# Kernel optimization log

Measured on AMD Instinct MI355X. Metric: run time of the kernel, lower is better.

## Reference

```python
import jax, jax.numpy as jnp
import numpy as np

B, D_IN, U, M = 8192, 512, 256, 50  # batch, input_size, num_units(=v_size), max_n_msgs


def _w(key, shape, scale=0.02):
    return (jax.random.normal(key, shape, dtype=jnp.float32) * scale)


def setup_inputs() -> dict:
    key = jax.random.key(0)
    ks = jax.random.split(key, 32)
    inp = {
        "X": jax.random.normal(ks[0], (B, D_IN), dtype=jnp.float32),
        "S": jax.random.normal(ks[1], (B, M, U), dtype=jnp.float32),
        "h": jax.random.normal(ks[2], (B, U), dtype=jnp.float32),
        "v": jax.random.normal(ks[3], (B, U), dtype=jnp.float32),
        # attention params
        "W_sa": _w(ks[4], (U, U)), "W_ha": _w(ks[5], (U, U)),
        "b_a": jnp.zeros((U,), jnp.float32), "v_a": _w(ks[6], (U,)),
        # gates
        "W_f": _w(ks[7], (U, U)), "W_hf": _w(ks[8], (U, U)), "b_f": jnp.zeros((U,), jnp.float32),
        "W_o": _w(ks[9], (U, U)), "W_ho": _w(ks[10], (U, U)), "b_o": jnp.zeros((U,), jnp.float32),
        "W_t": _w(ks[11], (U, U)), "W_ht": _w(ks[12], (U, U)), "b_t": jnp.zeros((U,), jnp.float32),
        "W_k": _w(ks[13], (D_IN, U)), "W_hk": _w(ks[14], (U, U)), "W_vk": _w(ks[15], (U, U)), "b_k": jnp.zeros((U,), jnp.float32),
        "W_s": _w(ks[16], (D_IN, U)), "W_hs": _w(ks[17], (U, U)), "b_s": jnp.zeros((U,), jnp.float32),
        "W_v": _w(ks[18], (U, U)), "W_hv": _w(ks[19], (U, U)), "b_v": jnp.zeros((U,), jnp.float32),
    }
    return inp


def reference(X, S, h, v,
              W_sa, W_ha, b_a, v_a,
              W_f, W_hf, b_f,
              W_o, W_ho, b_o,
              W_t, W_ht, b_t,
              W_k, W_hk, W_vk, b_k,
              W_s, W_hs, b_s,
              W_v, W_hv, b_v):
    # additive attention over messages: a [B, M, U]
    a = jnp.tanh(jnp.einsum('bmv,vu->bmu', S, W_sa) + (h @ W_ha + b_a)[:, None, :])
    scores = jnp.einsum('bmu,u->bm', a, v_a)            # [B, M]
    P = jax.nn.softmax(scores, axis=1)                  # [B, M]
    text = jnp.einsum('bm,bmv->bv', P, S)               # [B, U]
    # LSTM-like gates
    F = jax.nn.sigmoid(text @ W_f + h @ W_hf + b_f)
    O = jax.nn.sigmoid(text @ W_o + h @ W_ho + b_o)
    text_new = jnp.tanh(text @ W_t + h @ W_ht + b_t)
    V = F * v + O * text_new                            # [B, U]
    k = jax.nn.sigmoid(X @ W_k + h @ W_hk + V @ W_vk + b_k)
    hx = jnp.tanh(X @ W_s + h @ W_hs + b_s)
    hv = jnp.tanh(V @ W_v + h @ W_hv + b_v)
    H = (1.0 - k) * hv + k * hx                         # [B, U]
    # original returns (H, P, MSINStateTuple(H, V)); new_state.h == H
    return (H, P, V)
```

## Files before the change

### kernel.cpp

```cpp
#include <hip/hip_runtime.h>
#include <cstddef>

typedef __bf16 bf16x8 __attribute__((ext_vector_type(8)));
typedef unsigned short u16x8 __attribute__((ext_vector_type(8)));
typedef float f32x4 __attribute__((ext_vector_type(4)));

#define B_N 8192
#define M_N 50
#define R_N (B_N * M_N)
#define P_OFF ((size_t)B_N * 256)
#define V_OFF ((size_t)B_N * 256 + (size_t)B_N * 50)
#define NBAT 16
#define NBLK (B_N / NBAT)

__device__ __forceinline__ float bf2f(unsigned short u) {
  return __uint_as_float(((unsigned int)u) << 16);
}
__device__ __forceinline__ unsigned short f2bf(float f) {
  unsigned int u = __float_as_uint(f);
  u += 0x7fffu + ((u >> 16) & 1u);
  return (unsigned short)(u >> 16);
}
__device__ __forceinline__ float fsig(float x) { return 1.f / (1.f + __expf(-x)); }
__device__ __forceinline__ float ftanh(float x) {
  float e = __expf(2.f * x);
  return 1.f - 2.f / (e + 1.f);
}

__device__ __forceinline__ float ld_ext(const void* p, size_t i, bool f32) {
  return f32 ? ((const float*)p)[i] : bf2f(((const unsigned short*)p)[i]);
}

__device__ __forceinline__ void gload_lds16(const void* g, void* l) {
  __builtin_amdgcn_global_load_lds(
      (const __attribute__((address_space(1))) unsigned int*)g,
      (__attribute__((address_space(3))) unsigned int*)l, 16, 0, 0);
}

__device__ __forceinline__ unsigned swz(unsigned a) {
  return a ^ (((a >> 7) & 7u) << 4);
}

__global__ void probe_dtype(const void* __restrict__ X, int* __restrict__ flag) {
  const int lane = threadIdx.x;
  const unsigned short u = ((const unsigned short*)X)[lane * 2];
  const int e = (u >> 7) & 0xff;
  const bool plausible = (e >= 110 && e <= 144) || (u == 0);
  const unsigned long long m = __ballot(plausible);
  if (lane == 0) *flag = (__popcll(m) < 32) ? 1 : 0;
}

struct TJobs {
  const void* src[15];
  unsigned short* dst[15];
  int K[15];
};

__global__ __launch_bounds__(256) void transpose_weights(TJobs jobs, const int* __restrict__ flagp) {
  const bool f32 = *flagp != 0;
  const int z = blockIdx.z;
  const void* __restrict__ src = jobs.src[z];
  unsigned short* __restrict__ dst = jobs.dst[z];
  const int K = jobs.K[z];
  const int k0 = blockIdx.y * 16;
  if (k0 >= K) return;
  const int n0 = blockIdx.x * 16;
  __shared__ __align__(16) unsigned short tile[16][17];
  const int tx = threadIdx.x & 15, ty = threadIdx.x >> 4;
  const size_t sidx = (size_t)(k0 + ty) * 256 + n0 + tx;
  tile[ty][tx] = f32 ? f2bf(((const float*)src)[sidx]) : ((const unsigned short*)src)[sidx];
  __syncthreads();
  dst[(size_t)(n0 + ty) * K + k0 + tx] = tile[tx][ty];
}

struct GJob {
  const void* A[3];
  const unsigned short* Wt[3];
  int K[3];
  int atag[3];
  const void* bias;
  const unsigned short* add;
  unsigned short* out;
  int act;
};
struct GJobs { GJob j[4]; };

__global__ __launch_bounds__(256) void gemm_small(GJobs jobs, const int* __restrict__ flagp) {
  const bool flag32 = *flagp != 0;
  const GJob job = jobs.j[blockIdx.z];
  const int tid = threadIdx.x;
  const int row0 = blockIdx.x * 64;
  const int col0 = blockIdx.y * 128;
  __shared__ __align__(16) unsigned short As[2][64][40];
  __shared__ __align__(16) unsigned short Ws[2][128][40];

  f32x4 acc[2][4];
#pragma unroll
  for (int i = 0; i < 2; ++i)
#pragma unroll
    for (int j = 0; j < 4; ++j) acc[i][j] = (f32x4){0.f, 0.f, 0.f, 0.f};

  const int wave = tid >> 6, lane = tid & 63;
  const int wr = wave >> 1, wc = wave & 1;
  const int quad = lane >> 4, l16 = lane & 15;

  const void* Aseg[3]; const unsigned short* Wseg[3]; int Kseg[3]; bool Fseg[3];
  int nseg = 0, nt = 0, sbeg[4];
  sbeg[0] = 0;
  for (int p = 0; p < 3; ++p) {
    if (job.K[p] == 0) break;
    Aseg[nseg] = job.A[p]; Wseg[nseg] = job.Wt[p]; Kseg[nseg] = job.K[p];
    Fseg[nseg] = (job.atag[p] == 1) || (job.atag[p] == 2 && flag32);
    nt += job.K[p] / 32;
    ++nseg; sbeg[nseg] = nt;
  }

  const int rA = tid >> 2, cA = (tid & 3) * 8;
  const int rW = tid >> 2, cW = (tid & 3) * 8;

  uint4 pa, pw0, pw1;
  float4 fa, fb;
  bool pf32 = false;

  auto issue = [&](int t) {
    int s = 0;
    while (t >= sbeg[s + 1]) ++s;
    const int k0 = (t - sbeg[s]) * 32;
    const int Kp = Kseg[s];
    pf32 = Fseg[s];
    if (pf32) {
      const float* fp = (const float*)Aseg[s] + (size_t)(row0 + rA) * Kp + k0 + cA;
      fa = *(const float4*)fp;
      fb = *(const float4*)(fp + 4);
    } else {
      pa = *(const uint4*)((const unsigned short*)Aseg[s] + (size_t)(row0 + rA) * Kp + k0 + cA);
    }
    pw0 = *(const uint4*)&Wseg[s][(size_t)(col0 + rW) * Kp + k0 + cW];
    pw1 = *(const uint4*)&Wseg[s][(size_t)(col0 + rW + 64) * Kp + k0 + cW];
  };
  auto commit = [&](int buf) {
    if (pf32) {
      u16x8 v;
      v[0] = f2bf(fa.x); v[1] = f2bf(fa.y); v[2] = f2bf(fa.z); v[3] = f2bf(fa.w);
      v[4] = f2bf(fb.x); v[5] = f2bf(fb.y); v[6] = f2bf(fb.z); v[7] = f2bf(fb.w);
      *(u16x8*)&As[buf][rA][cA] = v;
    } else {
      *(uint4*)&As[buf][rA][cA] = pa;
    }
    *(uint4*)&Ws[buf][rW][cW] = pw0;
    *(uint4*)&Ws[buf][rW + 64][cW] = pw1;
  };

  issue(0);
  commit(0);
  __syncthreads();

  int buf = 0;
  for (int t = 0; t < nt; ++t) {
    if (t + 1 < nt) issue(t + 1);
    bf16x8 af[2], bfr[4];
#pragma unroll
    for (int mi = 0; mi < 2; ++mi)
      af[mi] = *(const bf16x8*)&As[buf][wr * 32 + mi * 16 + l16][quad * 8];
#pragma unroll
    for (int ni = 0; ni < 4; ++ni)
      bfr[ni] = *(const bf16x8*)&Ws[buf][wc * 64 + ni * 16 + l16][quad * 8];
#pragma unroll
    for (int mi = 0; mi < 2; ++mi)
#pragma unroll
      for (int ni = 0; ni < 4; ++ni)
        acc[mi][ni] = __builtin_amdgcn_mfma_f32_16x16x32_bf16(af[mi], bfr[ni], acc[mi][ni], 0, 0, 0);
    if (t + 1 < nt) commit(buf ^ 1);
    __syncthreads();
    buf ^= 1;
  }

#pragma unroll
  for (int mi = 0; mi < 2; ++mi) {
#pragma unroll
    for (int ni = 0; ni < 4; ++ni) {
      const int col = col0 + wc * 64 + ni * 16 + l16;
      const float bias = job.bias ? ld_ext(job.bias, col, flag32) : 0.f;
      const int rowb = row0 + wr * 32 + mi * 16 + quad * 4;
#pragma unroll
      for (int r = 0; r < 4; ++r) {
        float v = acc[mi][ni][r] + bias;
        const size_t idx = (size_t)(rowb + r) * 256 + col;
        if (job.add) v += bf2f(job.add[idx]);
        if (job.act == 1) v = fsig(v);
        else if (job.act == 2) v = ftanh(v);
        job.out[idx] = f2bf(v);
      }
    }
  }
}

__global__ __launch_bounds__(512, 4) void attn_fused(
    const void* __restrict__ S,
    const unsigned short* __restrict__ WsaT,
    const unsigned short* __restrict__ hWa,
    const void* __restrict__ v_a,
    float* __restrict__ out,
    unsigned short* __restrict__ text,
    const int* __restrict__ flagp) {
  const bool f32 = *flagp != 0;
  const int tid = threadIdx.x;
  const int wave = tid >> 6, lane = tid & 63;
  const int quad = lane >> 4, l16 = lane & 15;
  const int col0 = wave * 32;

  __shared__ __align__(128) unsigned short Sl[2][8 * 64 * 32];
  __shared__ __align__(16) float red[64][8];
  __shared__ float Pl[64];
  __shared__ __align__(16) float tpart[2][256];

  bf16x8 wf[8][2];
#pragma unroll
  for (int kk = 0; kk < 8; ++kk)
#pragma unroll
    for (int ni = 0; ni < 2; ++ni)
      wf[kk][ni] = *(const bf16x8*)&WsaT[(size_t)(col0 + ni * 16 + l16) * 256 + kk * 32 + quad * 8];

  const float va0 = ld_ext(v_a, col0 + l16, f32);
  const float va1 = ld_ext(v_a, col0 + 16 + l16, f32);

  const int b0 = blockIdx.x * NBAT;

  auto stage = [&](int b, int buf) {
#pragma unroll
    for (int i = 0; i < 4; ++i) {
      const unsigned c = (unsigned)tid * 16 + i * 8192;
      const unsigned sl = c >> 12;
      const unsigned l = swz(c & 4095);
      const unsigned row = l >> 6;
      const unsigned ke = sl * 32 + ((l & 63) >> 1);
      const size_t g = ((size_t)b * 50 + (row < 50 ? row : 49)) * 256 + ke;
      if (f32) {
        const float* fp = (const float*)S + g;
        const float4 a = *(const float4*)fp;
        const float4 bb = *(const float4*)(fp + 4);
        u16x8 v;
        v[0] = f2bf(a.x); v[1] = f2bf(a.y); v[2] = f2bf(a.z); v[3] = f2bf(a.w);
        v[4] = f2bf(bb.x); v[5] = f2bf(bb.y); v[6] = f2bf(bb.z); v[7] = f2bf(bb.w);
        *(u16x8*)((char*)Sl[buf] + c) = v;
      } else {
        gload_lds16((const unsigned short*)S + g,
                    (char*)Sl[buf] + (wave << 10) + i * 8192);
      }
    }
  };

  stage(b0, 0);
  __syncthreads();

  for (int bi = 0; bi < NBAT; ++bi) {
    const int b = b0 + bi;
    const int buf = bi & 1;
    if (bi + 1 < NBAT) stage(b + 1, buf ^ 1);

    const float hw0 = bf2f(hWa[(size_t)b * 256 + col0 + l16]);
    const float hw1 = bf2f(hWa[(size_t)b * 256 + col0 + 16 + l16]);

    const char* sl = (const char*)Sl[buf];
    f32x4 acc[4][2];
#pragma unroll
    for (int mi = 0; mi < 4; ++mi) {
      acc[mi][0] = (f32x4){0.f, 0.f, 0.f, 0.f};
      acc[mi][1] = (f32x4){0.f, 0.f, 0.f, 0.f};
    }
#pragma unroll
    for (int kk = 0; kk < 8; ++kk) {
#pragma unroll
      for (int mi = 0; mi < 4; ++mi) {
        const bf16x8 af = *(const bf16x8*)(sl + kk * 4096 +
                              swz((unsigned)(mi * 16 + l16) * 64 + quad * 16));
        acc[mi][0] = __builtin_amdgcn_mfma_f32_16x16x32_bf16(af, wf[kk][0], acc[mi][0], 0, 0, 0);
        acc[mi][1] = __builtin_amdgcn_mfma_f32_16x16x32_bf16(af, wf[kk][1], acc[mi][1], 0, 0, 0);
      }
    }

#pragma unroll
    for (int mi = 0; mi < 4; ++mi) {
#pragma unroll
      for (int r = 0; r < 4; ++r) {
        float s = ftanh(acc[mi][0][r] + hw0) * va0 + ftanh(acc[mi][1][r] + hw1) * va1;
        s += __shfl_xor(s, 1);
        s += __shfl_xor(s, 2);
        s += __shfl_xor(s, 4);
        s += __shfl_xor(s, 8);
        if (l16 == 0) red[mi * 16 + quad * 4 + r][wave] = s;
      }
    }
    __syncthreads();

    if (tid < 64) {
      const float4* rp = (const float4*)red[tid];
      const float4 x = rp[0], y = rp[1];
      const float sc = x.x + x.y + x.z + x.w + y.x + y.y + y.z + y.w;
      float sv = (tid < 50) ? sc : -1e30f;
      float mx = sv;
#pragma unroll
      for (int off = 32; off > 0; off >>= 1) mx = fmaxf(mx, __shfl_xor(mx, off));
      float e = (tid < 50) ? __expf(sv - mx) : 0.f;
      float sum = e;
#pragma unroll
      for (int off = 32; off > 0; off >>= 1) sum += __shfl_xor(sum, off);
      const float p = e / sum;
      Pl[tid] = p;
      if (tid < 50) out[P_OFF + (size_t)b * 50 + tid] = p;
    }
    __syncthreads();

    {
      const int col = tid & 255, hh = tid >> 8;
      const unsigned slice = (unsigned)(col >> 5) * 4096;
      const unsigned bc = (unsigned)(col & 31) * 2;
      float a = 0.f;
      const int m0 = hh * 25;
#pragma unroll 5
      for (int m = m0; m < m0 + 25; ++m)
        a += Pl[m] * bf2f(*(const unsigned short*)(sl + slice + swz((unsigned)m * 64 + bc)));
      tpart[hh][col] = a;
    }
    __syncthreads();
    if (tid < 256)
      text[(size_t)b * 256 + tid] = f2bf(tpart[0][tid] + tpart[1][tid]);
  }
}

__global__ __launch_bounds__(256) void v_combine(
    const unsigned short* __restrict__ F, const unsigned short* __restrict__ O,
    const unsigned short* __restrict__ T,
    const void* __restrict__ v, float* __restrict__ out,
    const int* __restrict__ flagp) {
  const bool f32 = *flagp != 0;
  const int i = (blockIdx.x * 256 + threadIdx.x) * 4;
  float v0, v1, v2, v3;
  if (f32) {
    const float4 vv = *(const float4*)((const float*)v + i);
    v0 = vv.x; v1 = vv.y; v2 = vv.z; v3 = vv.w;
  } else {
    const uint2 vr = *(const uint2*)((const unsigned short*)v + i);
    v0 = bf2f((unsigned short)(vr.x & 0xffffu));
    v1 = bf2f((unsigned short)(vr.x >> 16));
    v2 = bf2f((unsigned short)(vr.y & 0xffffu));
    v3 = bf2f((unsigned short)(vr.y >> 16));
  }
  const uint2 Fr = *(const uint2*)&F[i];
  const uint2 Or = *(const uint2*)&O[i];
  const uint2 Tr = *(const uint2*)&T[i];
  float4 o;
  o.x = bf2f((unsigned short)(Fr.x & 0xffffu)) * v0 + bf2f((unsigned short)(Or.x & 0xffffu)) * bf2f((unsigned short)(Tr.x & 0xffffu));
  o.y = bf2f((unsigned short)(Fr.x >> 16))     * v1 + bf2f((unsigned short)(Or.x >> 16))     * bf2f((unsigned short)(Tr.x >> 16));
  o.z = bf2f((unsigned short)(Fr.y & 0xffffu)) * v2 + bf2f((unsigned short)(Or.y & 0xffffu)) * bf2f((unsigned short)(Tr.y & 0xffffu));
  o.w = bf2f((unsigned short)(Fr.y >> 16))     * v3 + bf2f((unsigned short)(Or.y >> 16))     * bf2f((unsigned short)(Tr.y >> 16));
  *(float4*)&out[V_OFF + i] = o;
}

__global__ __launch_bounds__(256) void h_combine(
    const unsigned short* __restrict__ kk, const unsigned short* __restrict__ hv,
    const unsigned short* __restrict__ hx, float* __restrict__ Hout) {
  const int i = (blockIdx.x * 256 + threadIdx.x) * 4;
  const uint2 kr = *(const uint2*)&kk[i];
  const uint2 vr = *(const uint2*)&hv[i];
  const uint2 xr = *(const uint2*)&hx[i];
  const float k0 = bf2f((unsigned short)(kr.x & 0xffffu)), k1 = bf2f((unsigned short)(kr.x >> 16));
  const float k2 = bf2f((unsigned short)(kr.y & 0xffffu)), k3 = bf2f((unsigned short)(kr.y >> 16));
  const float hv0 = bf2f((unsigned short)(vr.x & 0xffffu)), hv1 = bf2f((unsigned short)(vr.x >> 16));
  const float hv2 = bf2f((unsigned short)(vr.y & 0xffffu)), hv3 = bf2f((unsigned short)(vr.y >> 16));
  const float hx0 = bf2f((unsigned short)(xr.x & 0xffffu)), hx1 = bf2f((unsigned short)(xr.x >> 16));
  const float hx2 = bf2f((unsigned short)(xr.y & 0xffffu)), hx3 = bf2f((unsigned short)(xr.y >> 16));
  float4 o;
  o.x = (1.f - k0) * hv0 + k0 * hx0;
  o.y = (1.f - k1) * hv1 + k1 * hx1;
  o.z = (1.f - k2) * hv2 + k2 * hx2;
  o.w = (1.f - k3) * hv3 + k3 * hx3;
  *(float4*)&Hout[i] = o;
}

extern "C" void kernel_launch(void* const* d_in, const int* in_sizes, int n_in,
                              void* d_out, int out_size, void* d_ws, size_t ws_size,
                              hipStream_t stream) {
  const void* X   = d_in[0];
  const void* S   = d_in[1];
  const void* h   = d_in[2];
  const void* v   = d_in[3];
  const void* b_a = d_in[6];
  const void* v_a = d_in[7];
  const void* b_f = d_in[10];
  const void* b_o = d_in[13];
  const void* b_t = d_in[16];
  const void* b_k = d_in[20];
  const void* b_s = d_in[23];
  const void* b_v = d_in[26];

  float* out = (float*)d_out;
  float* out_V = out + V_OFF;

  char* ws = (char*)d_ws;
  int* flag = (int*)ws;
  size_t off = 256;

  const int widx[15] = {4, 5, 8, 9, 11, 12, 14, 15, 17, 18, 19, 21, 22, 24, 25};
  const int wK[15]   = {256, 256, 256, 256, 256, 256, 256, 256, 512, 256, 256, 512, 256, 256, 256};
  TJobs tj;
  unsigned short* wt[15];
  for (int i = 0; i < 15; ++i) {
    wt[i] = (unsigned short*)(ws + off);
    off += (size_t)wK[i] * 256 * 2;
    tj.src[i] = d_in[widx[i]];
    tj.dst[i] = wt[i];
    tj.K[i] = wK[i];
  }
  const unsigned short *WsaT = wt[0], *WhaT = wt[1], *WfT = wt[2], *WhfT = wt[3],
                       *WoT = wt[4], *WhoT = wt[5], *WtT = wt[6], *WhtT = wt[7],
                       *WkT = wt[8], *WhkT = wt[9], *WvkT = wt[10], *WsT = wt[11],
                       *WhsT = wt[12], *WvT = wt[13], *WhvT = wt[14];
  off = (off + 255) & ~(size_t)255;
  const size_t BS = (size_t)B_N * 256 * 2;
  unsigned short* hWa   = (unsigned short*)(ws + off); off += BS;
  unsigned short* text  = (unsigned short*)(ws + off); off += BS;
  unsigned short* Fb    = (unsigned short*)(ws + off); off += BS;
  unsigned short* Ob    = (unsigned short*)(ws + off); off += BS;
  unsigned short* Tb    = (unsigned short*)(ws + off); off += BS;
  unsigned short* kpre  = (unsigned short*)(ws + off); off += BS;
  unsigned short* hx    = (unsigned short*)(ws + off); off += BS;
  unsigned short* hvpre = (unsigned short*)(ws + off); off += BS;

  probe_dtype<<<1, 64, 0, stream>>>(X, flag);
  transpose_weights<<<dim3(16, 32, 15), 256, 0, stream>>>(tj, flag);

  GJobs jA;
  for (int i = 0; i < 4; ++i) jA.j[i] = GJob{};
  jA.j[0].A[0] = h;  jA.j[0].atag[0] = 2; jA.j[0].Wt[0] = WhaT; jA.j[0].K[0] = 256;
  jA.j[0].bias = b_a; jA.j[0].out = hWa; jA.j[0].act = 0;
  jA.j[1].A[0] = X;  jA.j[1].atag[0] = 2; jA.j[1].Wt[0] = WkT;  jA.j[1].K[0] = 512;
  jA.j[1].A[1] = h;  jA.j[1].atag[1] = 2; jA.j[1].Wt[1] = WhkT; jA.j[1].K[1] = 256;
  jA.j[1].bias = b_k; jA.j[1].out = kpre; jA.j[1].act = 0;
  jA.j[2].A[0] = X;  jA.j[2].atag[0] = 2; jA.j[2].Wt[0] = WsT;  jA.j[2].K[0] = 512;
  jA.j[2].A[1] = h;  jA.j[2].atag[1] = 2; jA.j[2].Wt[1] = WhsT; jA.j[2].K[1] = 256;
  jA.j[2].bias = b_s; jA.j[2].out = hx; jA.j[2].act = 2;
  jA.j[3].A[0] = h;  jA.j[3].atag[0] = 2; jA.j[3].Wt[0] = WhvT; jA.j[3].K[0] = 256;
  jA.j[3].bias = b_v; jA.j[3].out = hvpre; jA.j[3].act = 0;
  gemm_small<<<dim3(128, 2, 4), 256, 0, stream>>>(jA, flag);

  attn_fused<<<dim3(NBLK), 512, 0, stream>>>(S, WsaT, hWa, v_a, out, text, flag);

  GJobs jB;
  for (int i = 0; i < 4; ++i) jB.j[i] = GJob{};
  jB.j[0].A[0] = text; jB.j[0].atag[0] = 0; jB.j[0].Wt[0] = WfT;  jB.j[0].K[0] = 256;
  jB.j[0].A[1] = h;    jB.j[0].atag[1] = 2; jB.j[0].Wt[1] = WhfT; jB.j[0].K[1] = 256;
  jB.j[0].bias = b_f; jB.j[0].out = Fb; jB.j[0].act = 1;
  jB.j[1].A[0] = text; jB.j[1].atag[0] = 0; jB.j[1].Wt[0] = WoT;  jB.j[1].K[0] = 256;
  jB.j[1].A[1] = h;    jB.j[1].atag[1] = 2; jB.j[1].Wt[1] = WhoT; jB.j[1].K[1] = 256;
  jB.j[1].bias = b_o; jB.j[1].out = Ob; jB.j[1].act = 1;
  jB.j[2].A[0] = text; jB.j[2].atag[0] = 0; jB.j[2].Wt[0] = WtT;  jB.j[2].K[0] = 256;
  jB.j[2].A[1] = h;    jB.j[2].atag[1] = 2; jB.j[2].Wt[1] = WhtT; jB.j[2].K[1] = 256;
  jB.j[2].bias = b_t; jB.j[2].out = Tb; jB.j[2].act = 2;
  gemm_small<<<dim3(128, 2, 3), 256, 0, stream>>>(jB, flag);

  v_combine<<<dim3(B_N * 256 / 1024), 256, 0, stream>>>(Fb, Ob, Tb, v, out, flag);

  GJobs jC;
  for (int i = 0; i < 4; ++i) jC.j[i] = GJob{};
  jC.j[0].A[0] = out_V; jC.j[0].atag[0] = 1; jC.j[0].Wt[0] = WvkT; jC.j[0].K[0] = 256;
  jC.j[0].add = kpre; jC.j[0].out = kpre; jC.j[0].act = 1;
  jC.j[1].A[0] = out_V; jC.j[1].atag[0] = 1; jC.j[1].Wt[0] = WvT;  jC.j[1].K[0] = 256;
  jC.j[1].add = hvpre; jC.j[1].out = hvpre; jC.j[1].act = 2;
  gemm_small<<<dim3(128, 2, 2), 256, 0, stream>>>(jC, flag);

  h_combine<<<dim3(B_N * 256 / 1024), 256, 0, stream>>>(kpre, hvpre, hx, out);
}
```

Before: 870.3 us.

## Use DPP reductions and single-wave global-read text accumulation in attention kernel

Replaces the shuffle-based 16-lane reductions of attention scores with DPP row adds and stores the per-wave partials as vector writes into a transposed reduction buffer. The softmax-weighted text sum now runs in a single wave that reads S directly from global memory in full precision, dropping the tpart buffer and one block barrier per batch row. Staging offsets are precomputed once, and in the bf16 path padding rows are no longer loaded. The trade-off is that one wave now serially does all of the text accumulation with global loads, which could become a per-iteration bottleneck.

```diff
diff --git a/kernel.cpp b/kernel.cpp
--- a/kernel.cpp
+++ b/kernel.cpp
@@ -39,6 +39,12 @@
 
 __device__ __forceinline__ unsigned swz(unsigned a) {
   return a ^ (((a >> 7) & 7u) << 4);
+}
+
+template <int CTRL>
+__device__ __forceinline__ float dpp_add(float v) {
+  return v + __int_as_float(
+      __builtin_amdgcn_update_dpp(0, __float_as_int(v), CTRL, 0xf, 0xf, true));
 }
 
 __global__ void probe_dtype(const void* __restrict__ X, int* __restrict__ flag) {
@@ -210,9 +216,8 @@
   const int col0 = wave * 32;
 
   __shared__ __align__(128) unsigned short Sl[2][8 * 64 * 32];
-  __shared__ __align__(16) float red[64][8];
+  __shared__ __align__(16) float red[8][64];
   __shared__ float Pl[64];
-  __shared__ __align__(16) float tpart[2][256];
 
   bf16x8 wf[8][2];
 #pragma unroll
@@ -226,26 +231,36 @@
 
   const int b0 = blockIdx.x * NBAT;
 
+  unsigned crow[4], goff[4];
+#pragma unroll
+  for (int i = 0; i < 4; ++i) {
+    const unsigned c = (unsigned)tid * 16 + i * 8192;
+    const unsigned sl = c >> 12;
+    const unsigned l = swz(c & 4095);
+    crow[i] = l >> 6;
+    goff[i] = (l >> 6) * 256 + sl * 32 + ((l & 63) >> 1);
+  }
+
   auto stage = [&](int b, int buf) {
-#pragma unroll
-    for (int i = 0; i < 4; ++i) {
-      const unsigned c = (unsigned)tid * 16 + i * 8192;
-      const unsigned sl = c >> 12;
-      const unsigned l = swz(c & 4095);
-      const unsigned row = l >> 6;
-      const unsigned ke = sl * 32 + ((l & 63) >> 1);
-      const size_t g = ((size_t)b * 50 + (row < 50 ? row : 49)) * 256 + ke;
-      if (f32) {
-        const float* fp = (const float*)S + g;
+    const size_t sbase = (size_t)b * (50 * 256);
+    if (f32) {
+#pragma unroll
+      for (int i = 0; i < 4; ++i) {
+        const unsigned row = crow[i] < 50 ? crow[i] : 49;
+        const float* fp = (const float*)S + sbase + row * 256 + (goff[i] - crow[i] * 256);
         const float4 a = *(const float4*)fp;
         const float4 bb = *(const float4*)(fp + 4);
         u16x8 v;
         v[0] = f2bf(a.x); v[1] = f2bf(a.y); v[2] = f2bf(a.z); v[3] = f2bf(a.w);
         v[4] = f2bf(bb.x); v[5] = f2bf(bb.y); v[6] = f2bf(bb.z); v[7] = f2bf(bb.w);
-        *(u16x8*)((char*)Sl[buf] + c) = v;
-      } else {
-        gload_lds16((const unsigned short*)S + g,
-                    (char*)Sl[buf] + (wave << 10) + i * 8192);
+        *(u16x8*)((char*)Sl[buf] + (unsigned)tid * 16 + i * 8192) = v;
+      }
+    } else {
+#pragma unroll
+      for (int i = 0; i < 4; ++i) {
+        if (crow[i] < 50)
+          gload_lds16((const unsigned short*)S + sbase + goff[i],
+                      (char*)Sl[buf] + (wave << 10) + i * 8192);
       }
     }
   };
@@ -281,50 +296,76 @@
 
 #pragma unroll
     for (int mi = 0; mi < 4; ++mi) {
+      f32x4 sv;
 #pragma unroll
       for (int r = 0; r < 4; ++r) {
-        float s = ftanh(acc[mi][0][r] + hw0) * va0 + ftanh(acc[mi][1][r] + hw1) * va1;
-        s += __shfl_xor(s, 1);
-        s += __shfl_xor(s, 2);
-        s += __shfl_xor(s, 4);
-        s += __shfl_xor(s, 8);
-        if (l16 == 0) red[mi * 16 + quad * 4 + r][wave] = s;
-      }
+        float t = ftanh(acc[mi][0][r] + hw0) * va0 + ftanh(acc[mi][1][r] + hw1) * va1;
+        t = dpp_add<0x128>(t);
+        t = dpp_add<0x124>(t);
+        t = dpp_add<0x122>(t);
+        t = dpp_add<0x121>(t);
+        sv[r] = t;
+      }
+      if (l16 == 0) *(f32x4*)&red[wave][mi * 16 + quad * 4] = sv;
     }
     __syncthreads();
 
-    if (tid < 64) {
-      const float4* rp = (const float4*)red[tid];
-      const float4 x = rp[0], y = rp[1];
-      const float sc = x.x + x.y + x.z + x.w + y.x + y.y + y.z + y.w;
-      float sv = (tid < 50) ? sc : -1e30f;
-      float mx = sv;
+    if (wave == 0) {
+      float s = 0.f;
+#pragma unroll
+      for (int w = 0; w < 8; ++w) s += red[w][lane];
+      float sv2 = (lane < 50) ? s : -1e30f;
+      float mx = sv2;
 #pragma unroll
       for (int off = 32; off > 0; off >>= 1) mx = fmaxf(mx, __shfl_xor(mx, off));
-      float e = (tid < 50) ? __expf(sv - mx) : 0.f;
+      float e = (lane < 50) ? __expf(sv2 - mx) : 0.f;
       float sum = e;
 #pragma unroll
       for (int off = 32; off > 0; off >>= 1) sum += __shfl_xor(sum, off);
       const float p = e / sum;
-      Pl[tid] = p;
-      if (tid < 50) out[P_OFF + (size_t)b * 50 + tid] = p;
+      Pl[lane] = p;
+      if (lane < 50) out[P_OFF + (size_t)b * 50 + lane] = p;
     }
     __syncthreads();
 
-    {
-      const int col = tid & 255, hh = tid >> 8;
-      const unsigned slice = (unsigned)(col >> 5) * 4096;
-      const unsigned bc = (unsigned)(col & 31) * 2;
-      float a = 0.f;
-      const int m0 = hh * 25;
+    if (wave == 1) {
+      const int c8 = lane >> 1, mh = lane & 1;
+      float tp[8];
+#pragma unroll
+      for (int e2 = 0; e2 < 8; ++e2) tp[e2] = 0.f;
+      const int m0 = mh * 25;
 #pragma unroll 5
-      for (int m = m0; m < m0 + 25; ++m)
-        a += Pl[m] * bf2f(*(const unsigned short*)(sl + slice + swz((unsigned)m * 64 + bc)));
-      tpart[hh][col] = a;
-    }
-    __syncthreads();
-    if (tid < 256)
-      text[(size_t)b * 256 + tid] = f2bf(tpart[0][tid] + tpart[1][tid]);
+      for (int j = 0; j < 25; ++j) {
+        const int m = m0 + j;
+        const float pm = Pl[m];
+        const size_t gi = ((size_t)b * 50 + m) * 256 + c8 * 8;
+        if (f32) {
+          const float* fp = (const float*)S + gi;
+          const float4 a = *(const float4*)fp;
+          const float4 bb = *(const float4*)(fp + 4);
+          tp[0] += pm * a.x;  tp[1] += pm * a.y;  tp[2] += pm * a.z;  tp[3] += pm * a.w;
+          tp[4] += pm * bb.x; tp[5] += pm * bb.y; tp[6] += pm * bb.z; tp[7] += pm * bb.w;
+        } else {
+          const uint4 raw = *(const uint4*)((const unsigned short*)S + gi);
+          tp[0] += pm * bf2f((unsigned short)(raw.x & 0xffffu));
+          tp[1] += pm * bf2f((unsigned short)(raw.x >> 16));
+          tp[2] += pm * bf2f((unsigned short)(raw.y & 0xffffu));
+          tp[3] += pm * bf2f((unsigned short)(raw.y >> 16));
+          tp[4] += pm * bf2f((unsigned short)(raw.z & 0xffffu));
+          tp[5] += pm * bf2f((unsigned short)(raw.z >> 16));
+          tp[6] += pm * bf2f((unsigned short)(raw.w & 0xffffu));
+          tp[7] += pm * bf2f((unsigned short)(raw.w >> 16));
+        }
+      }
+#pragma unroll
+      for (int e2 = 0; e2 < 8; ++e2) tp[e2] = dpp_add<0xB1>(tp[e2]);
+      if (mh == 0) {
+        u16x8 o;
+#pragma unroll
+        for (int e2 = 0; e2 < 8; ++e2) o[e2] = f2bf(tp[e2]);
+        *(u16x8*)&text[(size_t)b * 256 + c8 * 8] = o;
+      }
+    }
   }
 }
 
```

After: 974.7 us. +12.0%, slower.
